# Optimization experiments

Hardware: AMD Instinct MI355X
Metric: run time of the kernel (lower is better)

## Reference

```python
import jax, jax.numpy as jnp
import numpy as np

WS = 7          # window size
SHIFT = 3       # shift size = ws // 2
HEADS = 16
N = WS * WS     # tokens per window


def _rel_pos_index(ws):
    coords = np.stack(np.meshgrid(np.arange(ws), np.arange(ws), indexing='ij')).reshape(2, -1)
    rel = (coords[:, :, None] - coords[:, None, :]).transpose(1, 2, 0)
    rel[:, :, 0] += ws - 1
    rel[:, :, 1] += ws - 1
    rel[:, :, 0] *= 2 * ws - 1
    return rel.sum(-1)  # [N, N] int


def _attn_mask(H, W, ws, s):
    # Swin cyclic-shift mask: windows spanning the wrap boundary get -100 on
    # cross-region pairs so softmax zeroes them out.
    img = np.zeros((H, W), np.float32)
    cnt = 0
    for hs in (slice(0, -ws), slice(-ws, -s), slice(-s, None)):
        for wsl in (slice(0, -ws), slice(-ws, -s), slice(-s, None)):
            img[hs, wsl] = cnt
            cnt += 1
    mw = img.reshape(H // ws, ws, W // ws, ws).transpose(0, 2, 1, 3).reshape(-1, ws * ws)
    diff = mw[:, None, :] - mw[:, :, None]
    return np.where(diff != 0, np.float32(-100.0), np.float32(0.0))  # [nW, N, N]


def _window_partition(x, ws):
    B, H, W, C = x.shape
    x = x.reshape(B, H // ws, ws, W // ws, ws, C).transpose(0, 1, 3, 2, 4, 5)
    return x.reshape(-1, ws * ws, C)  # [B*nW, N, C]


def _window_reverse(x, ws, B, H, W):
    C = x.shape[-1]
    x = x.reshape(B, H // ws, W // ws, ws, ws, C).transpose(0, 1, 3, 2, 4, 5)
    return x.reshape(B, H, W, C)


def setup_inputs() -> dict:
    key = jax.random.key(0)
    ks = jax.random.split(key, 5)
    B, H, W, C = 16, 56, 56, 512
    x = jax.random.normal(ks[0], (B, H, W, C), jnp.float32)
    qkv_w = jax.random.normal(ks[1], (C, 3 * C), jnp.float32) * 0.02
    qkv_b = jnp.zeros((3 * C,), jnp.float32)
    proj_w = jax.random.normal(ks[2], (C, C), jnp.float32) * 0.02
    proj_b = jnp.zeros((C,), jnp.float32)
    rel_bias_table = jax.random.normal(ks[3], ((2 * WS - 1) ** 2, HEADS), jnp.float32) * 0.02
    return {"x": x, "qkv_w": qkv_w, "qkv_b": qkv_b,
            "proj_w": proj_w, "proj_b": proj_b, "rel_bias_table": rel_bias_table}


def reference(x, qkv_w, qkv_b, proj_w, proj_b, rel_bias_table):
    B, H, W, C = x.shape
    d = C // HEADS
    scale = jnp.float32(d) ** -0.5

    rel_idx = jnp.asarray(_rel_pos_index(WS))                 # [N, N]
    mask = jnp.asarray(_attn_mask(H, W, WS, SHIFT))           # [nW, N, N]
    nW = mask.shape[0]

    shortcut = x
    # cyclic shift
    xs = jnp.roll(x, shift=(-SHIFT, -SHIFT), axis=(1, 2))
    xw = _window_partition(xs, WS)                            # [B*nW, N, C]

    qkv = xw @ qkv_w + qkv_b                                  # [B*nW, N, 3C]
    qkv = qkv.reshape(-1, N, 3, HEADS, d).transpose(2, 0, 3, 1, 4)
    q, k, v = qkv[0], qkv[1], qkv[2]                          # each [B*nW, h, N, d]

    attn = jnp.einsum('whnd,whmd->whnm', q * scale, k)        # [B*nW, h, N, N]
    # gathered relative-position bias [h, N, N]
    bias = rel_bias_table[rel_idx.reshape(-1)].reshape(N, N, HEADS).transpose(2, 0, 1)
    attn = attn + bias[None]
    # shift mask, broadcast per window
    attn = attn.reshape(B, nW, HEADS, N, N) + mask[None, :, None]
    attn = jax.nn.softmax(attn.reshape(-1, HEADS, N, N), axis=-1)

    out = jnp.einsum('whnm,whmd->whnd', attn, v)              # [B*nW, h, N, d]
    out = out.transpose(0, 2, 1, 3).reshape(-1, N, C)
    out = out @ proj_w + proj_b

    out = _window_reverse(out, WS, B, H, W)
    out = jnp.roll(out, shift=(SHIFT, SHIFT), axis=(1, 2))
    return shortcut + out
```

## Files before the change

### kernel.cpp

```cpp
#include <hip/hip_runtime.h>
#include <stdint.h>

typedef unsigned short u16;
typedef unsigned int   u32;

typedef __bf16 bf16x8 __attribute__((ext_vector_type(8)));
typedef float  f32x4  __attribute__((ext_vector_type(4)));

__device__ __forceinline__ float bf2f(u16 h) {
    return __uint_as_float(((u32)h) << 16);
}
__device__ __forceinline__ u16 f2bf(float f) {
    u32 u = __float_as_uint(f);
    u += 0x7FFFu + ((u >> 16) & 1u);
    return (u16)(u >> 16);
}

#define GLOAD_LDS16(g, l)                                                     \
    __builtin_amdgcn_global_load_lds(                                         \
        (const __attribute__((address_space(1))) void*)(g),                   \
        (__attribute__((address_space(3))) void*)(l), 16, 0, 0)

__global__ __launch_bounds__(256) void cvt_f32_bf16(const float* __restrict__ in,
                                                    u16* __restrict__ out) {
    int i = blockIdx.x * 256 + threadIdx.x;
    const float4* p = (const float4*)in + (size_t)i * 2;
    float4 a = p[0], b = p[1];
    union { u16 s[8]; uint4 v; } o;
    o.s[0] = f2bf(a.x); o.s[1] = f2bf(a.y); o.s[2] = f2bf(a.z); o.s[3] = f2bf(a.w);
    o.s[4] = f2bf(b.x); o.s[5] = f2bf(b.y); o.s[6] = f2bf(b.z); o.s[7] = f2bf(b.w);
    ((uint4*)out)[i] = o.v;
}

__global__ void transpose_cvt(const float* __restrict__ in, u16* __restrict__ out,
                              int R, int Cc) {
    __shared__ float tile[32][33];
    int c0 = blockIdx.x * 32, r0 = blockIdx.y * 32;
    int tx = threadIdx.x, ty = threadIdx.y;
    tile[ty][tx] = in[(size_t)(r0 + ty) * Cc + c0 + tx];
    __syncthreads();
    out[(size_t)(c0 + ty) * R + r0 + tx] = f2bf(tile[tx][ty]);
}

__global__ __launch_bounds__(64) void build_bias(const float* __restrict__ table,
                                                 float* __restrict__ biasL) {
    int cls = blockIdx.x >> 4;
    int h   = blockIdx.x & 15;
    int lane = threadIdx.x;
    int quad = lane >> 4, l16 = lane & 15;
    int eh = cls >> 1, ew = cls & 1;
    float* base = biasL + (size_t)(cls * 16 + h) * 4096;
#pragma unroll
    for (int mi = 0; mi < 4; mi++) {
#pragma unroll
        for (int ni = 0; ni < 4; ni++) {
            float4 v;
            float* vp = &v.x;
#pragma unroll
            for (int r = 0; r < 4; r++) {
                int m = mi * 16 + quad * 4 + r;
                int c = ni * 16 + l16;
                float b;
                if (c >= 49)      b = -1e9f;
                else if (m >= 49) b = 0.f;
                else {
                    int ty = m / 7, tx = m % 7, jy = c / 7, jx = c % 7;
                    b = table[((ty - jy + 6) * 13 + (tx - jx + 6)) * 16 + h];
                    int ridr = (eh ? (ty < 4 ? 1 : 2) : 0) * 3 + (ew ? (tx < 4 ? 1 : 2) : 0);
                    int ridc = (eh ? (jy < 4 ? 1 : 2) : 0) * 3 + (ew ? (jx < 4 ? 1 : 2) : 0);
                    if (ridr != ridc) b -= 100.f;
                }
                vp[r] = b;
            }
            ((float4*)base)[((mi * 4 + ni) * 4 + quad) * 16 + l16] = v;
        }
    }
}

template <bool OUT_F32>
__global__ __launch_bounds__(512, 2) void gemm256(
    const u16* __restrict__ A, const u16* __restrict__ Bt,
    const float* __restrict__ bias, const float* __restrict__ res,
    void* __restrict__ Cout, int M, int N, int K, int GX)
{
    __shared__ __align__(16) char smem[131072];
    char* AsB = smem;
    char* BsB = smem + 65536;

    const int nwg = (int)gridDim.x;
    int wg = (int)blockIdx.x;
    wg = (wg & 7) * (nwg >> 3) + (wg >> 3);
    const int bx = wg % GX;
    const int by = wg / GX;
    const size_t m0 = (size_t)by * 256;
    const size_t n0 = (size_t)bx * 256;

    const int t    = threadIdx.x;
    const int lane = t & 63;
    const int w    = t >> 6;
    const int wm   = w >> 2, wn = w & 3;
    const int quad = lane >> 4, l16 = lane & 15;
    const int xr   = l16 & 7;
    const int cb   = (quad ^ xr) * 16;

    const int r0  = t >> 3;
    const int s8  = t & 7;
    const int swz = (s8 ^ (r0 & 7)) * 8;
    const u16* Ag0 = A  + (m0 + r0) * K + swz;
    const u16* Bg0 = Bt + (n0 + r0) * K + swz;
    const size_t j64K = (size_t)64 * K;
    const int lo0 = t * 16, lo1 = t * 16 + 8192;

    auto stageA = [&](int bf, int half, int ktt) {
        char* d = AsB + bf * 32768 + half * 16384;
        const u16* g = Ag0 + (size_t)half * 128 * K + ktt * 64;
        GLOAD_LDS16(g, d + lo0);
        GLOAD_LDS16(g + j64K, d + lo1);
    };
    auto stageB = [&](int bf, int half, int ktt) {
        char* d = BsB + bf * 32768 + half * 16384;
        const u16* g = Bg0 + (size_t)half * 128 * K + ktt * 64;
        GLOAD_LDS16(g, d + lo0);
        GLOAD_LDS16(g + j64K, d + lo1);
    };

    f32x4 acc[8][4];
    const f32x4 fz = {0.f, 0.f, 0.f, 0.f};
#pragma unroll
    for (int i = 0; i < 8; i++)
#pragma unroll
        for (int j = 0; j < 4; j++) acc[i][j] = fz;

    const int NT = K >> 6;

    stageA(0, 0, 0); stageA(0, 1, 0); stageB(0, 0, 0); stageB(0, 1, 0);
    stageB(1, 0, 1); stageA(1, 0, 1);
    asm volatile("s_waitcnt vmcnt(4)" ::: "memory");
    __builtin_amdgcn_s_barrier();

    for (int kt = 0; kt < NT; ++kt) {
        const int buf = kt & 1;
        const char* Ab  = AsB + buf * 32768 + wm * 16384 + l16 * 128;
        const char* Bb  = BsB + buf * 32768 + (wn >> 1) * 16384 + (wn & 1) * 8192 + l16 * 128;
        const char* pA0 = Ab + cb;
        const char* pA1 = Ab + (cb ^ 64);
        const char* pB0 = Bb + cb;
        const char* pB1 = Bb + (cb ^ 64);

        bf16x8 a[4][2], b0[2][2], b1[2][2];

#pragma unroll
        for (int mi = 0; mi < 4; mi++) {
            a[mi][0] = *(const bf16x8*)(pA0 + mi * 2048);
            a[mi][1] = *(const bf16x8*)(pA1 + mi * 2048);
        }
#pragma unroll
        for (int nj = 0; nj < 2; nj++) {
            b0[nj][0] = *(const bf16x8*)(pB0 + nj * 2048);
            b0[nj][1] = *(const bf16x8*)(pB1 + nj * 2048);
        }
        if (kt + 1 < NT) stageA((kt + 1) & 1, 1, kt + 1);
        __builtin_amdgcn_s_barrier();
        asm volatile("s_waitcnt lgkmcnt(0)" ::: "memory");
        __builtin_amdgcn_s_setprio(1);
#pragma unroll
        for (int mi = 0; mi < 4; mi++)
#pragma unroll
            for (int nj = 0; nj < 2; nj++) {
                acc[mi][nj] = __builtin_amdgcn_mfma_f32_16x16x32_bf16(
                    a[mi][0], b0[nj][0], acc[mi][nj], 0, 0, 0);
                acc[mi][nj] = __builtin_amdgcn_mfma_f32_16x16x32_bf16(
                    a[mi][1], b0[nj][1], acc[mi][nj], 0, 0, 0);
            }
        __builtin_amdgcn_s_setprio(0);
        __builtin_amdgcn_s_barrier();

#pragma unroll
        for (int nj = 0; nj < 2; nj++) {
            b1[nj][0] = *(const bf16x8*)(pB0 + 4096 + nj * 2048);
            b1[nj][1] = *(const bf16x8*)(pB1 + 4096 + nj * 2048);
        }
        if (kt + 1 < NT) stageB((kt + 1) & 1, 1, kt + 1);
        __builtin_amdgcn_s_barrier();
        asm volatile("s_waitcnt lgkmcnt(0)" ::: "memory");
        __builtin_amdgcn_s_setprio(1);
#pragma unroll
        for (int mi = 0; mi < 4; mi++)
#pragma unroll
            for (int nj = 0; nj < 2; nj++) {
                acc[mi][2 + nj] = __builtin_amdgcn_mfma_f32_16x16x32_bf16(
                    a[mi][0], b1[nj][0], acc[mi][2 + nj], 0, 0, 0);
                acc[mi][2 + nj] = __builtin_amdgcn_mfma_f32_16x16x32_bf16(
                    a[mi][1], b1[nj][1], acc[mi][2 + nj], 0, 0, 0);
            }
        __builtin_amdgcn_s_setprio(0);
        __builtin_amdgcn_s_barrier();

#pragma unroll
        for (int mi = 0; mi < 4; mi++) {
            a[mi][0] = *(const bf16x8*)(pA0 + 8192 + mi * 2048);
            a[mi][1] = *(const bf16x8*)(pA1 + 8192 + mi * 2048);
        }
        if (kt + 2 < NT) stageB(buf, 0, kt + 2);
        __builtin_amdgcn_s_barrier();
        asm volatile("s_waitcnt lgkmcnt(0)" ::: "memory");
        __builtin_amdgcn_s_setprio(1);
#pragma unroll
        for (int mi = 0; mi < 4; mi++)
#pragma unroll
            for (int nj = 0; nj < 2; nj++) {
                acc[4 + mi][2 + nj] = __builtin_amdgcn_mfma_f32_16x16x32_bf16(
                    a[mi][0], b1[nj][0], acc[4 + mi][2 + nj], 0, 0, 0);
                acc[4 + mi][2 + nj] = __builtin_amdgcn_mfma_f32_16x16x32_bf16(
                    a[mi][1], b1[nj][1], acc[4 + mi][2 + nj], 0, 0, 0);
            }
        __builtin_amdgcn_s_setprio(0);
        __builtin_amdgcn_s_barrier();

        if (kt + 2 < NT) stageA(buf, 0, kt + 2);
        __builtin_amdgcn_s_barrier();
        __builtin_amdgcn_s_setprio(1);
#pragma unroll
        for (int mi = 0; mi < 4; mi++)
#pragma unroll
            for (int nj = 0; nj < 2; nj++) {
                acc[4 + mi][nj] = __builtin_amdgcn_mfma_f32_16x16x32_bf16(
                    a[mi][0], b0[nj][0], acc[4 + mi][nj], 0, 0, 0);
                acc[4 + mi][nj] = __builtin_amdgcn_mfma_f32_16x16x32_bf16(
                    a[mi][1], b0[nj][1], acc[4 + mi][nj], 0, 0, 0);
            }
        __builtin_amdgcn_s_setprio(0);
        if (kt < NT - 2) asm volatile("s_waitcnt vmcnt(4)" ::: "memory");
        else             asm volatile("s_waitcnt vmcnt(0)" ::: "memory");
        __builtin_amdgcn_s_barrier();
    }

    float* scr = (float*)(void*)smem + w * 1088;
    float bv[4];
#pragma unroll
    for (int nj = 0; nj < 4; nj++)
        bv[nj] = bias[n0 + wn * 64 + nj * 16 + l16];

    const size_t colb = n0 + wn * 64 + quad * 16;
#pragma unroll
    for (int mi = 0; mi < 8; mi++) {
#pragma unroll
        for (int nj = 0; nj < 4; nj++)
#pragma unroll
            for (int r = 0; r < 4; r++)
                scr[(quad * 4 + r) * 68 + nj * 16 + l16] = acc[mi][nj][r] + bv[nj];
        asm volatile("s_waitcnt lgkmcnt(0)" ::: "memory");

        const size_t row = m0 + wm * 128 + mi * 16 + l16;
        const float4* sp = (const float4*)(scr + l16 * 68 + quad * 16);
        float4 v0 = sp[0], v1 = sp[1], v2 = sp[2], v3 = sp[3];

        if (OUT_F32) {
            const float4* rp = (const float4*)(res + row * N + colb);
            float4 r0v = rp[0], r1v = rp[1], r2v = rp[2], r3v = rp[3];
            v0.x += r0v.x; v0.y += r0v.y; v0.z += r0v.z; v0.w += r0v.w;
            v1.x += r1v.x; v1.y += r1v.y; v1.z += r1v.z; v1.w += r1v.w;
            v2.x += r2v.x; v2.y += r2v.y; v2.z += r2v.z; v2.w += r2v.w;
            v3.x += r3v.x; v3.y += r3v.y; v3.z += r3v.z; v3.w += r3v.w;
            float4* op = (float4*)((float*)Cout + row * N + colb);
            op[0] = v0; op[1] = v1; op[2] = v2; op[3] = v3;
        } else {
            union { u16 s[8]; uint4 q; } p0, p1;
            p0.s[0] = f2bf(v0.x); p0.s[1] = f2bf(v0.y); p0.s[2] = f2bf(v0.z); p0.s[3] = f2bf(v0.w);
            p0.s[4] = f2bf(v1.x); p0.s[5] = f2bf(v1.y); p0.s[6] = f2bf(v1.z); p0.s[7] = f2bf(v1.w);
            p1.s[0] = f2bf(v2.x); p1.s[1] = f2bf(v2.y); p1.s[2] = f2bf(v2.z); p1.s[3] = f2bf(v2.w);
            p1.s[4] = f2bf(v3.x); p1.s[5] = f2bf(v3.y); p1.s[6] = f2bf(v3.z); p1.s[7] = f2bf(v3.w);
            uint4* op = (uint4*)((u16*)Cout + row * N + colb);
            op[0] = p0.q; op[1] = p1.q;
        }
        asm volatile("s_waitcnt lgkmcnt(0)" ::: "memory");
    }
}

__global__ __launch_bounds__(64) void attn_kernel(
    const u16* __restrict__ qkv, const float* __restrict__ biasL,
    u16* __restrict__ O)
{
    __shared__ __align__(16) u16 Ps[64 * 72];
    __shared__ __align__(16) u16 Vts[32 * 72];

    const int wid = blockIdx.x >> 4;
    const int h   = blockIdx.x & 15;
    const int b   = wid >> 6;
    const int wy  = (wid >> 3) & 7;
    const int wx  = wid & 7;
    const int cls = ((wy == 7) ? 2 : 0) + ((wx == 7) ? 1 : 0);
    const int lane = threadIdx.x;
    const int quad = lane >> 4, l16 = lane & 15;

    auto tokOf = [&](int m) -> size_t {
        int tt = m < 49 ? m : 48;
        int ty = tt / 7, tx = tt - ty * 7;
        int ho = wy * 7 + ty + 3; if (ho >= 56) ho -= 56;
        int wo = wx * 7 + tx + 3; if (wo >= 56) wo -= 56;
        return ((size_t)b * 56 + ho) * 56 + wo;
    };

    {
        size_t tok = tokOf(lane);
        const uint4* vs = (const uint4*)(qkv + tok * 1536 + 1024 + h * 32);
        union { uint4 u4[4]; u16 s[32]; } vb;
        vb.u4[0] = vs[0]; vb.u4[1] = vs[1]; vb.u4[2] = vs[2]; vb.u4[3] = vs[3];
#pragma unroll
        for (int d = 0; d < 32; d++) Vts[d * 72 + lane] = vb.s[d];
    }

    bf16x8 aq[4], bk[4];
#pragma unroll
    for (int i = 0; i < 4; i++) {
        size_t tok = tokOf(i * 16 + l16);
        const u16* base = qkv + tok * 1536 + h * 32 + quad * 8;
        aq[i] = *(const bf16x8*)base;
        bk[i] = *(const bf16x8*)(base + 512);
    }

    f32x4 acc[4][4];
    {
        const f32x4 fzz = {0.f, 0.f, 0.f, 0.f};
#pragma unroll
        for (int mi = 0; mi < 4; mi++)
#pragma unroll
            for (int ni = 0; ni < 4; ni++)
                acc[mi][ni] = __builtin_amdgcn_mfma_f32_16x16x32_bf16(
                    aq[mi], bk[ni], fzz, 0, 0, 0);
    }

    {
        const float scale = 0.17677669529663687f;
        const float* bp = biasL + (size_t)(cls * 16 + h) * 4096;
#pragma unroll
        for (int mi = 0; mi < 4; mi++)
#pragma unroll
            for (int ni = 0; ni < 4; ni++) {
                float4 bvv = ((const float4*)bp)[((mi * 4 + ni) * 4 + quad) * 16 + l16];
                const float* bvp = &bvv.x;
#pragma unroll
                for (int r = 0; r < 4; r++)
                    acc[mi][ni][r] = acc[mi][ni][r] * scale + bvp[r];
            }
    }

    float rinv[4][4];
    {
#pragma unroll
        for (int mi = 0; mi < 4; mi++)
#pragma unroll
            for (int r = 0; r < 4; r++) {
                float m0 = fmaxf(fmaxf(acc[mi][0][r], acc[mi][1][r]),
                                 fmaxf(acc[mi][2][r], acc[mi][3][r]));
                m0 = fmaxf(m0, __shfl_xor(m0, 1, 64));
                m0 = fmaxf(m0, __shfl_xor(m0, 2, 64));
                m0 = fmaxf(m0, __shfl_xor(m0, 4, 64));
                m0 = fmaxf(m0, __shfl_xor(m0, 8, 64));
                float e0 = __expf(acc[mi][0][r] - m0);
                float e1 = __expf(acc[mi][1][r] - m0);
                float e2 = __expf(acc[mi][2][r] - m0);
                float e3 = __expf(acc[mi][3][r] - m0);
                acc[mi][0][r] = e0; acc[mi][1][r] = e1;
                acc[mi][2][r] = e2; acc[mi][3][r] = e3;
                float s0 = (e0 + e1) + (e2 + e3);
                s0 += __shfl_xor(s0, 1, 64);
                s0 += __shfl_xor(s0, 2, 64);
                s0 += __shfl_xor(s0, 4, 64);
                s0 += __shfl_xor(s0, 8, 64);
                rinv[mi][r] = __builtin_amdgcn_rcpf(s0);
            }
    }

#pragma unroll
    for (int mi = 0; mi < 4; mi++)
#pragma unroll
        for (int ni = 0; ni < 4; ni++)
#pragma unroll
            for (int r = 0; r < 4; r++)
                Ps[(mi * 16 + quad * 4 + r) * 72 + ni * 16 + l16] =
                    f2bf(acc[mi][ni][r]);
    __syncthreads();

#pragma unroll
    for (int mi = 0; mi < 4; mi++) {
        f32x4 c0 = {0.f, 0.f, 0.f, 0.f}, c1 = {0.f, 0.f, 0.f, 0.f};
#pragma unroll
        for (int ks = 0; ks < 2; ks++) {
            bf16x8 a = *(const bf16x8*)(Ps + (mi * 16 + l16) * 72 + ks * 32 + quad * 8);
            bf16x8 b0 = *(const bf16x8*)(Vts + l16 * 72 + ks * 32 + quad * 8);
            bf16x8 b1 = *(const bf16x8*)(Vts + (16 + l16) * 72 + ks * 32 + quad * 8);
            c0 = __builtin_amdgcn_mfma_f32_16x16x32_bf16(a, b0, c0, 0, 0, 0);
            c1 = __builtin_amdgcn_mfma_f32_16x16x32_bf16(a, b1, c1, 0, 0, 0);
        }
#pragma unroll
        for (int r = 0; r < 4; r++) {
            int m = mi * 16 + quad * 4 + r;
            if (m < 49) {
                int ty = m / 7, tx = m - ty * 7;
                int ho = wy * 7 + ty + 3; if (ho >= 56) ho -= 56;
                int wo = wx * 7 + tx + 3; if (wo >= 56) wo -= 56;
                size_t tok = ((size_t)b * 56 + ho) * 56 + wo;
                u16* op = O + tok * 512 + h * 32 + l16;
                op[0]  = f2bf(c0[r] * rinv[mi][r]);
                op[16] = f2bf(c1[r] * rinv[mi][r]);
            }
        }
    }
}

extern "C" void kernel_launch(void* const* d_in, const int* in_sizes, int n_in,
                              void* d_out, int out_size, void* d_ws, size_t ws_size,
                              hipStream_t stream)
{
    const float* x      = (const float*)d_in[0];
    const float* qkv_w  = (const float*)d_in[1];
    const float* qkv_b  = (const float*)d_in[2];
    const float* proj_w = (const float*)d_in[3];
    const float* proj_b = (const float*)d_in[4];
    const float* table  = (const float*)d_in[5];
    float* out = (float*)d_out;

    const int M  = 16 * 56 * 56;
    const int Cd = 512, C3 = 1536;

    char* ws = (char*)d_ws;
    u16* QKV  = (u16*)ws;
    u16* Xb   = (u16*)(ws + (size_t)M * C3 * 2);
    u16* Obuf = Xb;
    u16* Wt1  = (u16*)(ws + (size_t)M * C3 * 2 + (size_t)M * Cd * 2);
    u16* Wt2  = Wt1 + (size_t)C3 * Cd;
    float* biasL = (float*)Wt1;

    cvt_f32_bf16<<<(M * Cd) / 2048, 256, 0, stream>>>(x, Xb);

    dim3 tb(32, 32);
    transpose_cvt<<<dim3(C3 / 32, Cd / 32), tb, 0, stream>>>(qkv_w, Wt1, Cd, C3);
    transpose_cvt<<<dim3(Cd / 32, Cd / 32), tb, 0, stream>>>(proj_w, Wt2, Cd, Cd);

    gemm256<false><<<dim3((M / 256) * (C3 / 256)), 512, 0, stream>>>(
        Xb, Wt1, qkv_b, nullptr, QKV, M, C3, Cd, C3 / 256);

    build_bias<<<dim3(64), 64, 0, stream>>>(table, biasL);

    attn_kernel<<<dim3(1024 * 16), 64, 0, stream>>>(QKV, biasL, Obuf);

    gemm256<true><<<dim3((M / 256) * (Cd / 256)), 512, 0, stream>>>(
        Obuf, Wt2, proj_b, x, out, M, Cd, Cd, Cd / 256);
}
```

Measured before the change: 455.4 us.

## Merge prep kernels and compute transposed scores in attention to cut shuffles

The three preprocessing launches (x to bf16 conversion plus two weight transpose-converts) are merged into one launch that dispatches on block index. In the attention kernel, QK^T is now computed as K·Q^T, so each query's scores lie along the lane-quad and register dimension. The softmax reduction then needs only two cross-quad shuffles per column group instead of four per row. P is written to LDS with packed 8-byte stores, and the row reciprocals go through a small shared array. The bias layout is transposed to match. This adds LDS traffic for rsum and changes the P-store access pattern.

```diff
diff --git a/kernel.cpp b/kernel.cpp
--- a/kernel.cpp
+++ b/kernel.cpp
@@ -21,50 +21,63 @@
         (const __attribute__((address_space(1))) void*)(g),                   \
         (__attribute__((address_space(3))) void*)(l), 16, 0, 0)
 
-__global__ __launch_bounds__(256) void cvt_f32_bf16(const float* __restrict__ in,
-                                                    u16* __restrict__ out) {
-    int i = blockIdx.x * 256 + threadIdx.x;
-    const float4* p = (const float4*)in + (size_t)i * 2;
-    float4 a = p[0], b = p[1];
-    union { u16 s[8]; uint4 v; } o;
-    o.s[0] = f2bf(a.x); o.s[1] = f2bf(a.y); o.s[2] = f2bf(a.z); o.s[3] = f2bf(a.w);
-    o.s[4] = f2bf(b.x); o.s[5] = f2bf(b.y); o.s[6] = f2bf(b.z); o.s[7] = f2bf(b.w);
-    ((uint4*)out)[i] = o.v;
-}
-
-__global__ void transpose_cvt(const float* __restrict__ in, u16* __restrict__ out,
-                              int R, int Cc) {
+__global__ __launch_bounds__(1024) void prep_kernel(
+    const float* __restrict__ x,      u16* __restrict__ Xb,
+    const float* __restrict__ qkv_w,  u16* __restrict__ Wt1,
+    const float* __restrict__ proj_w, u16* __restrict__ Wt2)
+{
     __shared__ float tile[32][33];
-    int c0 = blockIdx.x * 32, r0 = blockIdx.y * 32;
-    int tx = threadIdx.x, ty = threadIdx.y;
-    tile[ty][tx] = in[(size_t)(r0 + ty) * Cc + c0 + tx];
-    __syncthreads();
-    out[(size_t)(c0 + ty) * R + r0 + tx] = f2bf(tile[tx][ty]);
+    const int bid = blockIdx.x;
+    const int t   = threadIdx.x;
+
+    if (bid < 3136) {
+        int i = bid * 1024 + t;
+        const float4* p = (const float4*)x + (size_t)i * 2;
+        float4 a = p[0], b = p[1];
+        union { u16 s[8]; uint4 v; } o;
+        o.s[0] = f2bf(a.x); o.s[1] = f2bf(a.y); o.s[2] = f2bf(a.z); o.s[3] = f2bf(a.w);
+        o.s[4] = f2bf(b.x); o.s[5] = f2bf(b.y); o.s[6] = f2bf(b.z); o.s[7] = f2bf(b.w);
+        ((uint4*)Xb)[i] = o.v;
+    } else if (bid < 3136 + 768) {
+        int lb = bid - 3136;
+        int c0 = (lb % 48) * 32, r0 = (lb / 48) * 32;
+        int tx = t & 31, ty = t >> 5;
+        tile[ty][tx] = qkv_w[(size_t)(r0 + ty) * 1536 + c0 + tx];
+        __syncthreads();
+        Wt1[(size_t)(c0 + ty) * 512 + r0 + tx] = f2bf(tile[tx][ty]);
+    } else {
+        int lb = bid - 3904;
+        int c0 = (lb & 15) * 32, r0 = (lb >> 4) * 32;
+        int tx = t & 31, ty = t >> 5;
+        tile[ty][tx] = proj_w[(size_t)(r0 + ty) * 512 + c0 + tx];
+        __syncthreads();
+        Wt2[(size_t)(c0 + ty) * 512 + r0 + tx] = f2bf(tile[tx][ty]);
+    }
 }
 
 __global__ __launch_bounds__(64) void build_bias(const float* __restrict__ table,
-                                                 float* __restrict__ biasL) {
+                                                 float* __restrict__ biasT) {
     int cls = blockIdx.x >> 4;
     int h   = blockIdx.x & 15;
     int lane = threadIdx.x;
     int quad = lane >> 4, l16 = lane & 15;
     int eh = cls >> 1, ew = cls & 1;
-    float* base = biasL + (size_t)(cls * 16 + h) * 4096;
-#pragma unroll
-    for (int mi = 0; mi < 4; mi++) {
-#pragma unroll
-        for (int ni = 0; ni < 4; ni++) {
+    float* base = biasT + (size_t)(cls * 16 + h) * 4096;
+#pragma unroll
+    for (int ki = 0; ki < 4; ki++) {
+#pragma unroll
+        for (int nj = 0; nj < 4; nj++) {
             float4 v;
             float* vp = &v.x;
 #pragma unroll
             for (int r = 0; r < 4; r++) {
-                int m = mi * 16 + quad * 4 + r;
-                int c = ni * 16 + l16;
+                int k = ki * 16 + quad * 4 + r;
+                int m = nj * 16 + l16;
                 float b;
-                if (c >= 49)      b = -1e9f;
+                if (k >= 49)      b = -1e9f;
                 else if (m >= 49) b = 0.f;
                 else {
-                    int ty = m / 7, tx = m % 7, jy = c / 7, jx = c % 7;
+                    int ty = m / 7, tx = m % 7, jy = k / 7, jx = k % 7;
                     b = table[((ty - jy + 6) * 13 + (tx - jx + 6)) * 16 + h];
                     int ridr = (eh ? (ty < 4 ? 1 : 2) : 0) * 3 + (ew ? (tx < 4 ? 1 : 2) : 0);
                     int ridc = (eh ? (jy < 4 ? 1 : 2) : 0) * 3 + (ew ? (jx < 4 ? 1 : 2) : 0);
@@ -72,7 +85,7 @@
                 }
                 vp[r] = b;
             }
-            ((float4*)base)[((mi * 4 + ni) * 4 + quad) * 16 + l16] = v;
+            ((float4*)base)[((ki * 4 + nj) * 4 + quad) * 16 + l16] = v;
         }
     }
 }
@@ -278,11 +291,12 @@
 }
 
 __global__ __launch_bounds__(64) void attn_kernel(
-    const u16* __restrict__ qkv, const float* __restrict__ biasL,
+    const u16* __restrict__ qkv, const float* __restrict__ biasT,
     u16* __restrict__ O)
 {
     __shared__ __align__(16) u16 Ps[64 * 72];
     __shared__ __align__(16) u16 Vts[32 * 72];
+    __shared__ __align__(16) float rsumS[64];
 
     const int wid = blockIdx.x >> 4;
     const int h   = blockIdx.x & 15;
@@ -319,72 +333,71 @@
         bk[i] = *(const bf16x8*)(base + 512);
     }
 
+    const f32x4 fz = {0.f, 0.f, 0.f, 0.f};
+
     f32x4 acc[4][4];
-    {
-        const f32x4 fzz = {0.f, 0.f, 0.f, 0.f};
-#pragma unroll
-        for (int mi = 0; mi < 4; mi++)
-#pragma unroll
-            for (int ni = 0; ni < 4; ni++)
-                acc[mi][ni] = __builtin_amdgcn_mfma_f32_16x16x32_bf16(
-                    aq[mi], bk[ni], fzz, 0, 0, 0);
-    }
+#pragma unroll
+    for (int ki = 0; ki < 4; ki++)
+#pragma unroll
+        for (int nj = 0; nj < 4; nj++)
+            acc[ki][nj] = __builtin_amdgcn_mfma_f32_16x16x32_bf16(
+                bk[ki], aq[nj], fz, 0, 0, 0);
 
     {
         const float scale = 0.17677669529663687f;
-        const float* bp = biasL + (size_t)(cls * 16 + h) * 4096;
-#pragma unroll
-        for (int mi = 0; mi < 4; mi++)
-#pragma unroll
-            for (int ni = 0; ni < 4; ni++) {
-                float4 bvv = ((const float4*)bp)[((mi * 4 + ni) * 4 + quad) * 16 + l16];
+        const float* bp = biasT + (size_t)(cls * 16 + h) * 4096;
+#pragma unroll
+        for (int ki = 0; ki < 4; ki++)
+#pragma unroll
+            for (int nj = 0; nj < 4; nj++) {
+                float4 bvv = ((const float4*)bp)[((ki * 4 + nj) * 4 + quad) * 16 + l16];
                 const float* bvp = &bvv.x;
 #pragma unroll
                 for (int r = 0; r < 4; r++)
-                    acc[mi][ni][r] = acc[mi][ni][r] * scale + bvp[r];
-            }
-    }
-
-    float rinv[4][4];
-    {
-#pragma unroll
-        for (int mi = 0; mi < 4; mi++)
+                    acc[ki][nj][r] = acc[ki][nj][r] * scale + bvp[r];
+            }
+    }
+
+#pragma unroll
+    for (int nj = 0; nj < 4; nj++) {
+        float mx = acc[0][nj][0];
+#pragma unroll
+        for (int ki = 0; ki < 4; ki++)
+#pragma unroll
+            for (int r = 0; r < 4; r++)
+                mx = fmaxf(mx, acc[ki][nj][r]);
+        mx = fmaxf(mx, __shfl_xor(mx, 16, 64));
+        mx = fmaxf(mx, __shfl_xor(mx, 32, 64));
+        float s = 0.f;
+#pragma unroll
+        for (int ki = 0; ki < 4; ki++)
 #pragma unroll
             for (int r = 0; r < 4; r++) {
-                float m0 = fmaxf(fmaxf(acc[mi][0][r], acc[mi][1][r]),
-                                 fmaxf(acc[mi][2][r], acc[mi][3][r]));
-                m0 = fmaxf(m0, __shfl_xor(m0, 1, 64));
-                m0 = fmaxf(m0, __shfl_xor(m0, 2, 64));
-                m0 = fmaxf(m0, __shfl_xor(m0, 4, 64));
-                m0 = fmaxf(m0, __shfl_xor(m0, 8, 64));
-                float e0 = __expf(acc[mi][0][r] - m0);
-                float e1 = __expf(acc[mi][1][r] - m0);
-                float e2 = __expf(acc[mi][2][r] - m0);
-                float e3 = __expf(acc[mi][3][r] - m0);
-                acc[mi][0][r] = e0; acc[mi][1][r] = e1;
-                acc[mi][2][r] = e2; acc[mi][3][r] = e3;
-                float s0 = (e0 + e1) + (e2 + e3);
-                s0 += __shfl_xor(s0, 1, 64);
-                s0 += __shfl_xor(s0, 2, 64);
-                s0 += __shfl_xor(s0, 4, 64);
-                s0 += __shfl_xor(s0, 8, 64);
-                rinv[mi][r] = __builtin_amdgcn_rcpf(s0);
-            }
-    }
-
-#pragma unroll
-    for (int mi = 0; mi < 4; mi++)
-#pragma unroll
-        for (int ni = 0; ni < 4; ni++)
-#pragma unroll
-            for (int r = 0; r < 4; r++)
-                Ps[(mi * 16 + quad * 4 + r) * 72 + ni * 16 + l16] =
-                    f2bf(acc[mi][ni][r]);
+                float e = __expf(acc[ki][nj][r] - mx);
+                acc[ki][nj][r] = e;
+                s += e;
+            }
+        s += __shfl_xor(s, 16, 64);
+        s += __shfl_xor(s, 32, 64);
+        if (quad == 0) rsumS[nj * 16 + l16] = __builtin_amdgcn_rcpf(s);
+    }
+
+#pragma unroll
+    for (int ki = 0; ki < 4; ki++)
+#pragma unroll
+        for (int nj = 0; nj < 4; nj++) {
+            union { u16 s4[4]; uint2 v; } pk;
+            pk.s4[0] = f2bf(acc[ki][nj][0]);
+            pk.s4[1] = f2bf(acc[ki][nj][1]);
+            pk.s4[2] = f2bf(acc[ki][nj][2]);
+            pk.s4[3] = f2bf(acc[ki][nj][3]);
+            *(uint2*)(Ps + (nj * 16 + l16) * 72 + ki * 16 + quad * 4) = pk.v;
+        }
     __syncthreads();
 
 #pragma unroll
     for (int mi = 0; mi < 4; mi++) {
-        f32x4 c0 = {0.f, 0.f, 0.f, 0.f}, c1 = {0.f, 0.f, 0.f, 0.f};
+        f32x4 c0 = fz, c1 = fz;
 #pragma unroll
         for (int ks = 0; ks < 2; ks++) {
             bf16x8 a = *(const bf16x8*)(Ps + (mi * 16 + l16) * 72 + ks * 32 + quad * 8);
@@ -393,6 +406,7 @@
             c0 = __builtin_amdgcn_mfma_f32_16x16x32_bf16(a, b0, c0, 0, 0, 0);
             c1 = __builtin_amdgcn_mfma_f32_16x16x32_bf16(a, b1, c1, 0, 0, 0);
         }
+        f32x4 rv = *(const f32x4*)(rsumS + mi * 16 + quad * 4);
 #pragma unroll
         for (int r = 0; r < 4; r++) {
             int m = mi * 16 + quad * 4 + r;
@@ -402,8 +416,8 @@
                 int wo = wx * 7 + tx + 3; if (wo >= 56) wo -= 56;
                 size_t tok = ((size_t)b * 56 + ho) * 56 + wo;
                 u16* op = O + tok * 512 + h * 32 + l16;
-                op[0]  = f2bf(c0[r] * rinv[mi][r]);
-                op[16] = f2bf(c1[r] * rinv[mi][r]);
+                op[0]  = f2bf(c0[r] * rv[r]);
+                op[16] = f2bf(c1[r] * rv[r]);
             }
         }
     }
@@ -430,20 +444,16 @@
     u16* Obuf = Xb;
     u16* Wt1  = (u16*)(ws + (size_t)M * C3 * 2 + (size_t)M * Cd * 2);
     u16* Wt2  = Wt1 + (size_t)C3 * Cd;
-    float* biasL = (float*)Wt1;
-
-    cvt_f32_bf16<<<(M * Cd) / 2048, 256, 0, stream>>>(x, Xb);
-
-    dim3 tb(32, 32);
-    transpose_cvt<<<dim3(C3 / 32, Cd / 32), tb, 0, stream>>>(qkv_w, Wt1, Cd, C3);
-    transpose_cvt<<<dim3(Cd / 32, Cd / 32), tb, 0, stream>>>(proj_w, Wt2, Cd, Cd);
+    float* biasT = (float*)Wt1;
+
+    prep_kernel<<<dim3(4160), 1024, 0, stream>>>(x, Xb, qkv_w, Wt1, proj_w, Wt2);
 
     gemm256<false><<<dim3((M / 256) * (C3 / 256)), 512, 0, stream>>>(
         Xb, Wt1, qkv_b, nullptr, QKV, M, C3, Cd, C3 / 256);
 
-    build_bias<<<dim3(64), 64, 0, stream>>>(table, biasL);
-
-    attn_kernel<<<dim3(1024 * 16), 64, 0, stream>>>(QKV, biasL, Obuf);
+    build_bias<<<dim3(64), 64, 0, stream>>>(table, biasT);
+
+    attn_kernel<<<dim3(1024 * 16), 64, 0, stream>>>(QKV, biasT, Obuf);
 
     gemm256<true><<<dim3((M / 256) * (Cd / 256)), 512, 0, stream>>>(
         Obuf, Wt2, proj_b, x, out, M, Cd, Cd, Cd / 256);
```

Result: no change. 452.6 us (-0.6%).
